# Optimization experiments

Hardware: AMD Instinct MI355X
Metric: run time of the kernel (lower is better)

The kernel has to match this reference:

```python
import jax, jax.numpy as jnp
import numpy as np

EPS = 1e-5

def layer_norm(h, g, b):
    m = h.mean(-1, keepdims=True)
    v = ((h - m) ** 2).mean(-1, keepdims=True)
    return (h - m) * jax.lax.rsqrt(v + EPS) * g + b

def setup_inputs() -> dict:
    key = jax.random.key(0)
    ks = jax.random.split(key, 16)
    B, D, C, H, EH, L = 64, 20000, 16, 64, 128, 32
    s = lambda k, fan_in, shape: jax.random.normal(k, shape, jnp.float32) / np.sqrt(fan_in)
    return {
        "x": jax.random.normal(ks[0], (B, D), jnp.float32),
        "mask": jax.random.randint(ks[1], (B, D), 0, 2, jnp.int32),
        "feature_embedding": jax.random.normal(ks[2], (D, C), jnp.float32),
        # h_layer: Linear(1+C -> H), LN, ReLU, Linear(H -> C), LN, ReLU
        "W1": s(ks[3], 1 + C, (1 + C, H)), "b1": jnp.zeros((H,), jnp.float32),
        "g1": jnp.ones((H,), jnp.float32), "be1": jnp.zeros((H,), jnp.float32),
        "W2": s(ks[4], H, (H, C)), "b2": jnp.zeros((C,), jnp.float32),
        "g2": jnp.ones((C,), jnp.float32), "be2": jnp.zeros((C,), jnp.float32),
        # encoder_mlp (FCLayers, 2 layers, LayerNorm + ReLU each): C -> EH -> 2L
        "We1": s(ks[5], C, (C, EH)), "bb1": jnp.zeros((EH,), jnp.float32),
        "gg1": jnp.ones((EH,), jnp.float32), "bbe1": jnp.zeros((EH,), jnp.float32),
        "We2": s(ks[6], EH, (EH, 2 * L)), "bb2": jnp.zeros((2 * L,), jnp.float32),
        "gg2": jnp.ones((2 * L,), jnp.float32), "bbe2": jnp.zeros((2 * L,), jnp.float32),
    }

def reference(x, mask, feature_embedding, W1, b1, g1, be1, W2, b2, g2, be2,
              We1, bb1, gg1, bbe1, We2, bb2, gg2, bbe2):
    B, D = x.shape
    C = feature_embedding.shape[1]
    # per-feature point-net: h_layer runs row-wise, so we compute it densely
    # for all (b, d) and zero out unobserved entries before pooling —
    # identical math to the per-sample masked gather in the original.
    h_in = jnp.concatenate(
        [x[..., None], jnp.broadcast_to(feature_embedding, (B, D, C))], axis=-1
    )  # [B, D, 1+C]
    h = jax.nn.relu(layer_norm(h_in @ W1 + b1, g1, be1))   # [B, D, H]
    h = jax.nn.relu(layer_norm(h @ W2 + b2, g2, be2))      # [B, D, C]
    m = mask.astype(h.dtype)
    summed = jnp.einsum('bdc,bd->bc', h, m)                # masked sum pool
    num_obs = jnp.maximum(m.sum(axis=1, keepdims=True), 1.0)
    c = summed / num_obs                                   # pool_mode='mean'
    # encoder_mlp
    e = jax.nn.relu(layer_norm(c @ We1 + bb1, gg1, bbe1))
    e = jax.nn.relu(layer_norm(e @ We2 + bb2, gg2, bbe2))  # [B, 2*latent]
    mu, logvar = jnp.split(e, 2, axis=-1)
    return mu, logvar
```

## Files before the change

kernel.cpp:

```cpp
#include <hip/hip_runtime.h>
#include <hip/hip_bf16.h>

#define EPSF 1e-5f

namespace {
constexpr int B = 64, D = 20000, C = 16, H = 64, EH = 128, L = 32;
constexpr int DPAD = ((D + 63) / 64) * 64;
constexpr int NB = 1280;
constexpr int SSTRIDE = NB * 4;
constexpr int FB = 14;
constexpr int MAXU = B * (DPAD / 64);
}

typedef __attribute__((ext_vector_type(8))) short bf16x8;
typedef __attribute__((ext_vector_type(4))) float f32x4;
typedef __attribute__((ext_vector_type(2))) float f32x2;
typedef __attribute__((ext_vector_type(4))) unsigned int u32x4;

static __device__ __forceinline__ unsigned short f2bf(float f) {
    __hip_bfloat16 h = __float2bfloat16(f);
    return __builtin_bit_cast(unsigned short, h);
}
static __device__ __forceinline__ unsigned int packbf(float lo, float hi) {
    return ((unsigned int)f2bf(hi) << 16) | (unsigned int)f2bf(lo);
}
static __device__ __forceinline__ unsigned int cvtpk(float lo, float hi) {
    __hip_bfloat162 h2 = __float22bfloat162_rn(make_float2(lo, hi));
    return ((unsigned int)__builtin_bit_cast(unsigned short, h2.y) << 16)
         | (unsigned int)__builtin_bit_cast(unsigned short, h2.x);
}
static __device__ __forceinline__ f32x2 pk_fma(f32x2 a, f32x2 b, f32x2 c) {
    return __builtin_elementwise_fma(a, b, c);
}
static __device__ __forceinline__ f32x2 pk_add(f32x2 a, f32x2 b) { return a + b; }
static __device__ __forceinline__ f32x2 pk_mul(f32x2 a, f32x2 b) { return a * b; }

__global__ __launch_bounds__(1024) void k_prep(
    const int* __restrict__ mask, const float* __restrict__ x,
    const float* __restrict__ fe,
    const float* __restrict__ W1, const float* __restrict__ b1,
    const float* __restrict__ W2,
    int* __restrict__ cnt,
    unsigned short* __restrict__ cd, unsigned int* __restrict__ hxp,
    unsigned short* __restrict__ febf,
    unsigned short* __restrict__ W1T, unsigned short* __restrict__ W2T)
{
    const int t = threadIdx.x;
    if (blockIdx.x < B) {
        const int b = blockIdx.x;
        const size_t bD = (size_t)b * D;
        const size_t bP = (size_t)b * DPAD;
        constexpr int NIT = (D + 1023) / 1024;
        int   mv[NIT];
        float xv[NIT];
        #pragma unroll
        for (int it = 0; it < NIT; ++it) {
            const int d = it * 1024 + t;
            const bool in = d < D;
            mv[it] = in ? mask[bD + d] : 0;
            xv[it] = in ? x[bD + d] : 0.f;
        }
        int cl = 0;
        #pragma unroll
        for (int it = 0; it < NIT; ++it) cl += (mv[it] != 0) ? 1 : 0;

        const int lane = t & 63, wid = t >> 6;
        int inc = cl;
        #pragma unroll
        for (int off = 1; off < 64; off <<= 1) {
            const int v = __shfl_up(inc, off);
            if (lane >= off) inc += v;
        }
        __shared__ int ls[16];
        if (lane == 63) ls[wid] = inc;
        __syncthreads();
        int wbase = 0, tot = 0;
        #pragma unroll
        for (int k = 0; k < 16; ++k) {
            const int v = ls[k];
            tot += v;
            if (k < wid) wbase += v;
        }
        int pos = wbase + (inc - cl);

        #pragma unroll
        for (int it = 0; it < NIT; ++it) {
            if (mv[it]) {
                cd[bP + pos]  = (unsigned short)(it * 1024 + t);
                hxp[bP + pos] = packbf(xv[it], 1.0f);
                ++pos;
            }
        }
        const int padend = (tot + 63) & ~63;
        for (int i = tot + t; i < padend; i += 1024) {
            cd[bP + i] = 0;
            hxp[bP + i] = 0u;
        }
        if (t == 0) cnt[b] = tot;
    } else if (blockIdx.x == B) {
        for (int e = t; e < H * 32; e += 1024) {
            const int rIdx = e >> 5, kk = e & 31;
            const int m = rIdx >> 4, rho = rIdx & 15;
            const int h = 32 * (m >> 1) + 8 * (rho >> 2) + 4 * (m & 1) + (rho & 3);
            float v = 0.f;
            if (kk < 16)       v = W1[(kk + 1) * H + h];
            else if (kk == 16) v = W1[h];
            else if (kk == 17) v = b1[h];
            W1T[e] = f2bf(v);
        }
    } else if (blockIdx.x == B + 1) {
        for (int e = t; e < C * H; e += 1024) {
            const int c0 = e >> 6, hh = e & 63;
            W2T[e] = f2bf(W2[hh * C + c0]);
        }
    } else {
        const int pb = blockIdx.x - (B + 2);
        for (int u = pb * 1024 + t; u < (D * C) / 8; u += FB * 1024) {
            const float4 f0 = *(const float4*)(fe + (size_t)u * 8);
            const float4 f1 = *(const float4*)(fe + (size_t)u * 8 + 4);
            uint4 pk;
            pk.x = packbf(f0.x, f0.y); pk.y = packbf(f0.z, f0.w);
            pk.z = packbf(f1.x, f1.y); pk.w = packbf(f1.z, f1.w);
            *(uint4*)(febf + (size_t)u * 8) = pk;
        }
    }
}

static __device__ __forceinline__ void unit_it(
    const bf16x8& hbv, int rem, int pq,
    const bf16x8 (&w1f)[4], const bf16x8 (&w2f)[2],
    const f32x2 (&g1p)[4][2], const f32x2 (&be1p)[4][2],
    const f32x2& g2lo, const f32x2& g2hi,
    const f32x2& be2lo, const f32x2& be2hi,
    const f32x2& b2lo, const f32x2& b2hi,
    f32x2& laccLo, f32x2& laccHi)
{
    const f32x4 z = {0.f, 0.f, 0.f, 0.f};
    f32x4 t1a[4];
    #pragma unroll
    for (int m = 0; m < 4; ++m)
        t1a[m] = __builtin_amdgcn_mfma_f32_16x16x32_bf16(w1f[m], hbv, z, 0, 0, 0);

    f32x2 sp = {0.f, 0.f}, qp = {0.f, 0.f};
    f32x2 tl[4], th[4];
    #pragma unroll
    for (int m = 0; m < 4; ++m) {
        tl[m] = __builtin_shufflevector(t1a[m], t1a[m], 0, 1);
        th[m] = __builtin_shufflevector(t1a[m], t1a[m], 2, 3);
        sp = pk_add(sp, pk_add(tl[m], th[m]));
        qp = pk_fma(tl[m], tl[m], pk_fma(th[m], th[m], qp));
    }
    float s  = sp[0] + sp[1];
    float sq = qp[0] + qp[1];
    s  += __shfl_xor(s, 16);  sq += __shfl_xor(sq, 16);
    s  += __shfl_xor(s, 32);  sq += __shfl_xor(sq, 32);
    const float mean1 = s * (1.f / H);
    const float var1  = fmaxf(sq * (1.f / H) - mean1 * mean1, 0.f);
    const float rstd1 = rsqrtf(var1 + EPSF);

    const f32x2 rr2 = {rstd1, rstd1};
    const f32x2 nm2 = {-mean1, -mean1};
    unsigned int pw[8];
    #pragma unroll
    for (int m = 0; m < 4; ++m) {
        const f32x2 sgl = pk_mul(g1p[m][0], rr2);
        const f32x2 sgh = pk_mul(g1p[m][1], rr2);
        const f32x2 obl = pk_fma(sgl, nm2, be1p[m][0]);
        const f32x2 obh = pk_fma(sgh, nm2, be1p[m][1]);
        const f32x2 yl = pk_fma(tl[m], sgl, obl);
        const f32x2 yh = pk_fma(th[m], sgh, obh);
        pw[2 * m]     = cvtpk(fmaxf(yl[0], 0.f), fmaxf(yl[1], 0.f));
        pw[2 * m + 1] = cvtpk(fmaxf(yh[0], 0.f), fmaxf(yh[1], 0.f));
    }
    const u32x4 r0 = {pw[0], pw[1], pw[2], pw[3]};
    const u32x4 r1 = {pw[4], pw[5], pw[6], pw[7]};
    const bf16x8 rb0 = __builtin_bit_cast(bf16x8, r0);
    const bf16x8 rb1 = __builtin_bit_cast(bf16x8, r1);

    f32x4 a2 = __builtin_amdgcn_mfma_f32_16x16x32_bf16(w2f[0], rb0, z, 0, 0, 0);
    a2 = __builtin_amdgcn_mfma_f32_16x16x32_bf16(w2f[1], rb1, a2, 0, 0, 0);

    f32x2 alo = __builtin_shufflevector(a2, a2, 0, 1);
    f32x2 ahi = __builtin_shufflevector(a2, a2, 2, 3);
    alo = pk_add(alo, b2lo);
    ahi = pk_add(ahi, b2hi);
    const f32x2 sp2 = pk_add(alo, ahi);
    const f32x2 zz = {0.f, 0.f};
    const f32x2 qp2 = pk_fma(alo, alo, pk_fma(ahi, ahi, zz));
    float s2 = sp2[0] + sp2[1];
    float q2 = qp2[0] + qp2[1];
    s2 += __shfl_xor(s2, 16);  q2 += __shfl_xor(q2, 16);
    s2 += __shfl_xor(s2, 32);  q2 += __shfl_xor(q2, 32);
    const float mean2 = s2 * (1.f / C);
    const float var2  = fmaxf(q2 * (1.f / C) - mean2 * mean2, 0.f);
    const float rstd2 = rsqrtf(var2 + EPSF);

    const f32x2 rrb = {rstd2, rstd2};
    const f32x2 nmb = {-mean2, -mean2};
    const f32x2 sg2l = pk_mul(g2lo, rrb);
    const f32x2 sg2h = pk_mul(g2hi, rrb);
    const f32x2 ob2l = pk_fma(sg2l, nmb, be2lo);
    const f32x2 ob2h = pk_fma(sg2h, nmb, be2hi);
    const f32x2 y2l = pk_fma(alo, sg2l, ob2l);
    const f32x2 y2h = pk_fma(ahi, sg2h, ob2h);
    const float vm = (pq < rem) ? 1.f : 0.f;
    const f32x2 vm2 = {vm, vm};
    const f32x2 rl = {fmaxf(y2l[0], 0.f), fmaxf(y2l[1], 0.f)};
    const f32x2 rh = {fmaxf(y2h[0], 0.f), fmaxf(y2h[1], 0.f)};
    laccLo = pk_fma(rl, vm2, laccLo);
    laccHi = pk_fma(rh, vm2, laccHi);
}

__global__ __launch_bounds__(256, 2) void k_rows(
    const int* __restrict__ cnt,
    const unsigned short* __restrict__ cd, const unsigned int* __restrict__ hxp,
    const unsigned short* __restrict__ febf,
    const unsigned short* __restrict__ W1T, const unsigned short* __restrict__ W2T,
    const float* __restrict__ g1, const float* __restrict__ be1,
    const float* __restrict__ g2, const float* __restrict__ be2,
    const float* __restrict__ b2,
    float* __restrict__ part)
{
    const int tid = threadIdx.x;
    const int w = tid >> 6, lane = tid & 63;
    const int g = lane >> 4, q = lane & 15;

    const int cv  = cnt[lane];
    const int nuv = (cv + 63) >> 6;
    int Pi = nuv;
    #pragma unroll
    for (int off = 1; off < 64; off <<= 1) {
        const int pv = __shfl_up(Pi, off);
        if (lane >= off) Pi += pv;
    }
    const int T = __shfl(Pi, 63);

    const int uA = blockIdx.x * 4 + w;
    if (uA >= T) return;
    const bool hasB = (uA + SSTRIDE) < T;
    const int uB = hasB ? uA + SSTRIDE : uA;

    bf16x8 w1f[4];
    #pragma unroll
    for (int m = 0; m < 4; ++m)
        w1f[m] = *(const bf16x8*)(W1T + (16 * m + q) * 32 + 8 * g);
    bf16x8 w2f[2];
    #pragma unroll
    for (int ks = 0; ks < 2; ++ks)
        w2f[ks] = *(const bf16x8*)(W2T + q * 64 + 32 * ks + 8 * g);

    f32x2 g1p[4][2], be1p[4][2];
    #pragma unroll
    for (int m = 0; m < 4; ++m) {
        const int h0 = 32 * (m >> 1) + 8 * g + 4 * (m & 1);
        g1p[m][0]  = *(const f32x2*)(g1  + h0);
        g1p[m][1]  = *(const f32x2*)(g1  + h0 + 2);
        be1p[m][0] = *(const f32x2*)(be1 + h0);
        be1p[m][1] = *(const f32x2*)(be1 + h0 + 2);
    }
    const f32x2 g2lo  = *(const f32x2*)(g2  + 4 * g);
    const f32x2 g2hi  = *(const f32x2*)(g2  + 4 * g + 2);
    const f32x2 be2lo = *(const f32x2*)(be2 + 4 * g);
    const f32x2 be2hi = *(const f32x2*)(be2 + 4 * g + 2);
    const f32x2 b2lo  = *(const f32x2*)(b2  + 4 * g);
    const f32x2 b2hi  = *(const f32x2*)(b2  + 4 * g + 2);

    size_t rowbA, rowbB;
    int remA, remB;
    {
        const unsigned long long blA = __ballot(Pi <= uA);
        const int bA   = __popcll(blA);
        const int PbA  = __shfl(Pi, bA);
        const int nubA = __shfl(nuv, bA);
        const int nA   = __shfl(cv, bA);
        const int baseA = (uA - (PbA - nubA)) * 64;
        rowbA = (size_t)bA * DPAD + baseA;
        remA  = nA - baseA;
        const unsigned long long blB = __ballot(Pi <= uB);
        const int bB   = __popcll(blB);
        const int PbB  = __shfl(Pi, bB);
        const int nubB = __shfl(nuv, bB);
        const int nB   = __shfl(cv, bB);
        const int baseB = (uB - (PbB - nubB)) * 64;
        rowbB = (size_t)bB * DPAD + baseB;
        remB  = nB - baseB;
    }

    const int dvA = (int)cd[rowbA + lane];
    const int dvB = (int)cd[rowbB + lane];

    bf16x8 hbA[4], hbB[4];
    #pragma unroll
    for (int it = 0; it < 4; ++it) {
        const int p = (it << 4) + q;
        {
            const int dd = __shfl(dvA, p);
            bf16x8 hv = {0, 0, 0, 0, 0, 0, 0, 0};
            if (g < 2) {
                hv = *(const bf16x8*)(febf + (size_t)dd * 16 + 8 * g);
            } else if (g == 2) {
                const unsigned int xv = hxp[rowbA + p];
                const u32x4 tmp = {xv, 0u, 0u, 0u};
                hv = __builtin_bit_cast(bf16x8, tmp);
            }
            hbA[it] = hv;
        }
        {
            const int dd = __shfl(dvB, p);
            bf16x8 hv = {0, 0, 0, 0, 0, 0, 0, 0};
            if (g < 2) {
                hv = *(const bf16x8*)(febf + (size_t)dd * 16 + 8 * g);
            } else if (g == 2) {
                const unsigned int xv = hxp[rowbB + p];
                const u32x4 tmp = {xv, 0u, 0u, 0u};
                hv = __builtin_bit_cast(bf16x8, tmp);
            }
            hbB[it] = hv;
        }
    }

    f32x2 laLoA = {0.f, 0.f}, laHiA = {0.f, 0.f};
    f32x2 laLoB = {0.f, 0.f}, laHiB = {0.f, 0.f};
    #pragma unroll
    for (int it = 0; it < 4; ++it) {
        const int pq = (it << 4) + q;
        unit_it(hbA[it], remA, pq, w1f, w2f, g1p, be1p,
                g2lo, g2hi, be2lo, be2hi, b2lo, b2hi, laLoA, laHiA);
        unit_it(hbB[it], remB, pq, w1f, w2f, g1p, be1p,
                g2lo, g2hi, be2lo, be2hi, b2lo, b2hi, laLoB, laHiB);
    }

    float a0 = laLoA[0], a1 = laLoA[1], a2 = laHiA[0], a3 = laHiA[1];
    float b0 = laLoB[0], b1 = laLoB[1], b2v_ = laHiB[0], b3 = laHiB[1];
    #pragma unroll
    for (int off = 1; off < 16; off <<= 1) {
        a0 += __shfl_xor(a0, off);  a1 += __shfl_xor(a1, off);
        a2 += __shfl_xor(a2, off);  a3 += __shfl_xor(a3, off);
        b0 += __shfl_xor(b0, off);  b1 += __shfl_xor(b1, off);
        b2v_ += __shfl_xor(b2v_, off);  b3 += __shfl_xor(b3, off);
    }
    if (q == 0) {
        *(float4*)(part + (size_t)uA * C + 4 * g) = make_float4(a0, a1, a2, a3);
        if (hasB)
            *(float4*)(part + (size_t)uB * C + 4 * g) = make_float4(b0, b1, b2v_, b3);
    }
}

__global__ __launch_bounds__(EH) void k_enc(
    const float* __restrict__ part, const int* __restrict__ cnt,
    const float* __restrict__ We1, const float* __restrict__ bb1,
    const float* __restrict__ gg1, const float* __restrict__ bbe1,
    const float* __restrict__ We2, const float* __restrict__ bb2,
    const float* __restrict__ gg2, const float* __restrict__ bbe2,
    float* __restrict__ out)
{
    const int b = blockIdx.x;
    const int t = threadIdx.x;
    __shared__ int sP[64];
    __shared__ float red[8][16];
    __shared__ float cc[C];
    __shared__ float stats[2];
    __shared__ float buf[EH];
    __shared__ float buf2[2 * L];

    if (t < 64) {
        int p = (cnt[t] + 63) >> 6;
        #pragma unroll
        for (int off = 1; off < 64; off <<= 1) {
            const int pv = __shfl_up(p, off);
            if (t >= off) p += pv;
        }
        sP[t] = p;
    }
    __syncthreads();
    const int n = cnt[b];
    const int row0 = (b == 0) ? 0 : sP[b - 1];
    const int rows = sP[b] - row0;

    {
        const int c = t & 15, s = t >> 4;
        float ps = 0.f;
        for (int r = s; r < rows; r += 8)
            ps += part[(size_t)(row0 + r) * C + c];
        red[s][c] = ps;
    }
    __syncthreads();
    if (t < C) {
        float v = 0.f;
        #pragma unroll
        for (int s = 0; s < 8; ++s) v += red[s][t];
        cc[t] = v;
    }
    __syncthreads();
    const float inv = 1.f / fmaxf((float)n, 1.f);

    float v1 = bb1[t];
    #pragma unroll
    for (int c = 0; c < C; ++c)
        v1 = fmaf(cc[c] * inv, We1[c * EH + t], v1);
    buf[t] = v1;
    __syncthreads();
    if (t == 0) {
        float s = 0.f, ss = 0.f;
        for (int j2 = 0; j2 < EH; ++j2) { s += buf[j2]; ss = fmaf(buf[j2], buf[j2], ss); }
        float mn = s * (1.f / EH);
        float vr = fmaxf(ss * (1.f / EH) - mn * mn, 0.f);
        stats[0] = mn; stats[1] = rsqrtf(vr + EPSF);
    }
    __syncthreads();
    float e1 = fmaxf(fmaf((v1 - stats[0]) * stats[1], gg1[t], bbe1[t]), 0.f);
    __syncthreads();
    buf[t] = e1;
    __syncthreads();

    float v2 = 0.f;
    if (t < 2 * L) {
        v2 = bb2[t];
        #pragma unroll
        for (int h = 0; h < EH; ++h)
            v2 = fmaf(buf[h], We2[h * (2 * L) + t], v2);
        buf2[t] = v2;
    }
    __syncthreads();
    if (t == 0) {
        float s = 0.f, ss = 0.f;
        for (int j2 = 0; j2 < 2 * L; ++j2) { s += buf2[j2]; ss = fmaf(buf2[j2], buf2[j2], ss); }
        float mn = s * (1.f / (2 * L));
        float vr = fmaxf(ss * (1.f / (2 * L)) - mn * mn, 0.f);
        stats[0] = mn; stats[1] = rsqrtf(vr + EPSF);
    }
    __syncthreads();
    if (t < 2 * L) {
        float e2 = fmaxf(fmaf((v2 - stats[0]) * stats[1], gg2[t], bbe2[t]), 0.f);
        if (t < L) out[(size_t)b * L + t]                       = e2;
        else       out[(size_t)B * L + (size_t)b * L + (t - L)] = e2;
    }
}

extern "C" void kernel_launch(void* const* d_in, const int* in_sizes, int n_in,
                              void* d_out, int out_size, void* d_ws, size_t ws_size,
                              hipStream_t stream) {
    const float* x    = (const float*)d_in[0];
    const int*   mask = (const int*)d_in[1];
    const float* fe   = (const float*)d_in[2];
    const float* W1   = (const float*)d_in[3];
    const float* b1   = (const float*)d_in[4];
    const float* g1   = (const float*)d_in[5];
    const float* be1  = (const float*)d_in[6];
    const float* W2   = (const float*)d_in[7];
    const float* b2   = (const float*)d_in[8];
    const float* g2   = (const float*)d_in[9];
    const float* be2  = (const float*)d_in[10];
    const float* We1  = (const float*)d_in[11];
    const float* bb1  = (const float*)d_in[12];
    const float* gg1  = (const float*)d_in[13];
    const float* bbe1 = (const float*)d_in[14];
    const float* We2  = (const float*)d_in[15];
    const float* bb2  = (const float*)d_in[16];
    const float* gg2  = (const float*)d_in[17];
    const float* bbe2 = (const float*)d_in[18];
    float* out = (float*)d_out;

    char* wp = (char*)d_ws;
    float* part     = (float*)wp;               wp += (size_t)MAXU * C * 4;
    int*   cnt      = (int*)wp;                 wp += (size_t)B * 4;
    unsigned short* W1T = (unsigned short*)wp;  wp += (size_t)H * 32 * 2;
    unsigned short* W2T = (unsigned short*)wp;  wp += (size_t)C * H * 2;
    unsigned short* febf = (unsigned short*)wp; wp += (size_t)D * C * 2;
    unsigned int*   hxp = (unsigned int*)wp;    wp += (size_t)B * DPAD * 4;
    unsigned short* cd  = (unsigned short*)wp;

    hipLaunchKernelGGL(k_prep, dim3(B + 2 + FB), dim3(1024), 0, stream,
                       mask, x, fe, W1, b1, W2, cnt, cd, hxp, febf, W1T, W2T);
    hipLaunchKernelGGL(k_rows, dim3(NB), dim3(256), 0, stream,
                       cnt, cd, hxp, febf, W1T, W2T, g1, be1, g2, be2, b2, part);
    hipLaunchKernelGGL(k_enc, dim3(B), dim3(EH), 0, stream,
                       part, cnt, We1, bb1, gg1, bbe1, We2, bb2, gg2, bbe2, out);
}
```

Measured before the change: 47.67 us.

## Fuse prep, row, and encoder kernels into one persistent kernel with grid barriers

Merges the three kernel launches into a single persistent kernel of 512 blocks separated by two atomic-counter grid barriers, removing launch gaps between stages. The compaction stage now runs with 256-thread blocks using a ballot-based iterative scan instead of 1024-thread blocks. The row stage loops over units grid-stride instead of one-shot. It adds a memset launch, spin-wait overhead, and relies on all 512 blocks being co-resident (launch bounds allow 2 per CU). The per-batch compaction is now serialized over 79 iterations per block, which could lengthen the first stage.

```diff
diff --git a/kernel.cpp b/kernel.cpp
--- a/kernel.cpp
+++ b/kernel.cpp
@@ -6,9 +6,8 @@
 namespace {
 constexpr int B = 64, D = 20000, C = 16, H = 64, EH = 128, L = 32;
 constexpr int DPAD = ((D + 63) / 64) * 64;
-constexpr int NB = 1280;
-constexpr int SSTRIDE = NB * 4;
-constexpr int FB = 14;
+constexpr int NBF = 512;
+constexpr int WSTRIDE = NBF * 4;
 constexpr int MAXU = B * (DPAD / 64);
 }
 
@@ -35,95 +34,19 @@
 static __device__ __forceinline__ f32x2 pk_add(f32x2 a, f32x2 b) { return a + b; }
 static __device__ __forceinline__ f32x2 pk_mul(f32x2 a, f32x2 b) { return a * b; }
 
-__global__ __launch_bounds__(1024) void k_prep(
-    const int* __restrict__ mask, const float* __restrict__ x,
-    const float* __restrict__ fe,
-    const float* __restrict__ W1, const float* __restrict__ b1,
-    const float* __restrict__ W2,
-    int* __restrict__ cnt,
-    unsigned short* __restrict__ cd, unsigned int* __restrict__ hxp,
-    unsigned short* __restrict__ febf,
-    unsigned short* __restrict__ W1T, unsigned short* __restrict__ W2T)
-{
-    const int t = threadIdx.x;
-    if (blockIdx.x < B) {
-        const int b = blockIdx.x;
-        const size_t bD = (size_t)b * D;
-        const size_t bP = (size_t)b * DPAD;
-        constexpr int NIT = (D + 1023) / 1024;
-        int   mv[NIT];
-        float xv[NIT];
-        #pragma unroll
-        for (int it = 0; it < NIT; ++it) {
-            const int d = it * 1024 + t;
-            const bool in = d < D;
-            mv[it] = in ? mask[bD + d] : 0;
-            xv[it] = in ? x[bD + d] : 0.f;
-        }
-        int cl = 0;
-        #pragma unroll
-        for (int it = 0; it < NIT; ++it) cl += (mv[it] != 0) ? 1 : 0;
-
-        const int lane = t & 63, wid = t >> 6;
-        int inc = cl;
-        #pragma unroll
-        for (int off = 1; off < 64; off <<= 1) {
-            const int v = __shfl_up(inc, off);
-            if (lane >= off) inc += v;
-        }
-        __shared__ int ls[16];
-        if (lane == 63) ls[wid] = inc;
-        __syncthreads();
-        int wbase = 0, tot = 0;
-        #pragma unroll
-        for (int k = 0; k < 16; ++k) {
-            const int v = ls[k];
-            tot += v;
-            if (k < wid) wbase += v;
-        }
-        int pos = wbase + (inc - cl);
-
-        #pragma unroll
-        for (int it = 0; it < NIT; ++it) {
-            if (mv[it]) {
-                cd[bP + pos]  = (unsigned short)(it * 1024 + t);
-                hxp[bP + pos] = packbf(xv[it], 1.0f);
-                ++pos;
-            }
-        }
-        const int padend = (tot + 63) & ~63;
-        for (int i = tot + t; i < padend; i += 1024) {
-            cd[bP + i] = 0;
-            hxp[bP + i] = 0u;
-        }
-        if (t == 0) cnt[b] = tot;
-    } else if (blockIdx.x == B) {
-        for (int e = t; e < H * 32; e += 1024) {
-            const int rIdx = e >> 5, kk = e & 31;
-            const int m = rIdx >> 4, rho = rIdx & 15;
-            const int h = 32 * (m >> 1) + 8 * (rho >> 2) + 4 * (m & 1) + (rho & 3);
-            float v = 0.f;
-            if (kk < 16)       v = W1[(kk + 1) * H + h];
-            else if (kk == 16) v = W1[h];
-            else if (kk == 17) v = b1[h];
-            W1T[e] = f2bf(v);
-        }
-    } else if (blockIdx.x == B + 1) {
-        for (int e = t; e < C * H; e += 1024) {
-            const int c0 = e >> 6, hh = e & 63;
-            W2T[e] = f2bf(W2[hh * C + c0]);
-        }
-    } else {
-        const int pb = blockIdx.x - (B + 2);
-        for (int u = pb * 1024 + t; u < (D * C) / 8; u += FB * 1024) {
-            const float4 f0 = *(const float4*)(fe + (size_t)u * 8);
-            const float4 f1 = *(const float4*)(fe + (size_t)u * 8 + 4);
-            uint4 pk;
-            pk.x = packbf(f0.x, f0.y); pk.y = packbf(f0.z, f0.w);
-            pk.z = packbf(f1.x, f1.y); pk.w = packbf(f1.z, f1.w);
-            *(uint4*)(febf + (size_t)u * 8) = pk;
-        }
-    }
+static __device__ __forceinline__ void grid_barrier(int* bar, int target) {
+    __syncthreads();
+    if (threadIdx.x == 0) {
+        __threadfence();
+        atomicAdd(bar, 1);
+        int spins = 0;
+        while (atomicAdd(bar, 0) < target) {
+            __builtin_amdgcn_s_sleep(8);
+            if (++spins > (1 << 24)) break;
+        }
+        __threadfence();
+    }
+    __syncthreads();
 }
 
 static __device__ __forceinline__ void unit_it(
@@ -211,229 +134,311 @@
     laccHi = pk_fma(rh, vm2, laccHi);
 }
 
-__global__ __launch_bounds__(256, 2) void k_rows(
-    const int* __restrict__ cnt,
-    const unsigned short* __restrict__ cd, const unsigned int* __restrict__ hxp,
-    const unsigned short* __restrict__ febf,
-    const unsigned short* __restrict__ W1T, const unsigned short* __restrict__ W2T,
+__global__ __launch_bounds__(256, 2) void k_fused(
+    const int* __restrict__ mask, const float* __restrict__ x,
+    const float* __restrict__ fe,
+    const float* __restrict__ W1, const float* __restrict__ b1,
     const float* __restrict__ g1, const float* __restrict__ be1,
+    const float* __restrict__ W2, const float* __restrict__ b2,
     const float* __restrict__ g2, const float* __restrict__ be2,
-    const float* __restrict__ b2,
-    float* __restrict__ part)
-{
-    const int tid = threadIdx.x;
-    const int w = tid >> 6, lane = tid & 63;
-    const int g = lane >> 4, q = lane & 15;
-
-    const int cv  = cnt[lane];
-    const int nuv = (cv + 63) >> 6;
-    int Pi = nuv;
-    #pragma unroll
-    for (int off = 1; off < 64; off <<= 1) {
-        const int pv = __shfl_up(Pi, off);
-        if (lane >= off) Pi += pv;
-    }
-    const int T = __shfl(Pi, 63);
-
-    const int uA = blockIdx.x * 4 + w;
-    if (uA >= T) return;
-    const bool hasB = (uA + SSTRIDE) < T;
-    const int uB = hasB ? uA + SSTRIDE : uA;
-
-    bf16x8 w1f[4];
-    #pragma unroll
-    for (int m = 0; m < 4; ++m)
-        w1f[m] = *(const bf16x8*)(W1T + (16 * m + q) * 32 + 8 * g);
-    bf16x8 w2f[2];
-    #pragma unroll
-    for (int ks = 0; ks < 2; ++ks)
-        w2f[ks] = *(const bf16x8*)(W2T + q * 64 + 32 * ks + 8 * g);
-
-    f32x2 g1p[4][2], be1p[4][2];
-    #pragma unroll
-    for (int m = 0; m < 4; ++m) {
-        const int h0 = 32 * (m >> 1) + 8 * g + 4 * (m & 1);
-        g1p[m][0]  = *(const f32x2*)(g1  + h0);
-        g1p[m][1]  = *(const f32x2*)(g1  + h0 + 2);
-        be1p[m][0] = *(const f32x2*)(be1 + h0);
-        be1p[m][1] = *(const f32x2*)(be1 + h0 + 2);
-    }
-    const f32x2 g2lo  = *(const f32x2*)(g2  + 4 * g);
-    const f32x2 g2hi  = *(const f32x2*)(g2  + 4 * g + 2);
-    const f32x2 be2lo = *(const f32x2*)(be2 + 4 * g);
-    const f32x2 be2hi = *(const f32x2*)(be2 + 4 * g + 2);
-    const f32x2 b2lo  = *(const f32x2*)(b2  + 4 * g);
-    const f32x2 b2hi  = *(const f32x2*)(b2  + 4 * g + 2);
-
-    size_t rowbA, rowbB;
-    int remA, remB;
-    {
-        const unsigned long long blA = __ballot(Pi <= uA);
-        const int bA   = __popcll(blA);
-        const int PbA  = __shfl(Pi, bA);
-        const int nubA = __shfl(nuv, bA);
-        const int nA   = __shfl(cv, bA);
-        const int baseA = (uA - (PbA - nubA)) * 64;
-        rowbA = (size_t)bA * DPAD + baseA;
-        remA  = nA - baseA;
-        const unsigned long long blB = __ballot(Pi <= uB);
-        const int bB   = __popcll(blB);
-        const int PbB  = __shfl(Pi, bB);
-        const int nubB = __shfl(nuv, bB);
-        const int nB   = __shfl(cv, bB);
-        const int baseB = (uB - (PbB - nubB)) * 64;
-        rowbB = (size_t)bB * DPAD + baseB;
-        remB  = nB - baseB;
-    }
-
-    const int dvA = (int)cd[rowbA + lane];
-    const int dvB = (int)cd[rowbB + lane];
-
-    bf16x8 hbA[4], hbB[4];
-    #pragma unroll
-    for (int it = 0; it < 4; ++it) {
-        const int p = (it << 4) + q;
-        {
-            const int dd = __shfl(dvA, p);
-            bf16x8 hv = {0, 0, 0, 0, 0, 0, 0, 0};
-            if (g < 2) {
-                hv = *(const bf16x8*)(febf + (size_t)dd * 16 + 8 * g);
-            } else if (g == 2) {
-                const unsigned int xv = hxp[rowbA + p];
-                const u32x4 tmp = {xv, 0u, 0u, 0u};
-                hv = __builtin_bit_cast(bf16x8, tmp);
-            }
-            hbA[it] = hv;
-        }
-        {
-            const int dd = __shfl(dvB, p);
-            bf16x8 hv = {0, 0, 0, 0, 0, 0, 0, 0};
-            if (g < 2) {
-                hv = *(const bf16x8*)(febf + (size_t)dd * 16 + 8 * g);
-            } else if (g == 2) {
-                const unsigned int xv = hxp[rowbB + p];
-                const u32x4 tmp = {xv, 0u, 0u, 0u};
-                hv = __builtin_bit_cast(bf16x8, tmp);
-            }
-            hbB[it] = hv;
-        }
-    }
-
-    f32x2 laLoA = {0.f, 0.f}, laHiA = {0.f, 0.f};
-    f32x2 laLoB = {0.f, 0.f}, laHiB = {0.f, 0.f};
-    #pragma unroll
-    for (int it = 0; it < 4; ++it) {
-        const int pq = (it << 4) + q;
-        unit_it(hbA[it], remA, pq, w1f, w2f, g1p, be1p,
-                g2lo, g2hi, be2lo, be2hi, b2lo, b2hi, laLoA, laHiA);
-        unit_it(hbB[it], remB, pq, w1f, w2f, g1p, be1p,
-                g2lo, g2hi, be2lo, be2hi, b2lo, b2hi, laLoB, laHiB);
-    }
-
-    float a0 = laLoA[0], a1 = laLoA[1], a2 = laHiA[0], a3 = laHiA[1];
-    float b0 = laLoB[0], b1 = laLoB[1], b2v_ = laHiB[0], b3 = laHiB[1];
-    #pragma unroll
-    for (int off = 1; off < 16; off <<= 1) {
-        a0 += __shfl_xor(a0, off);  a1 += __shfl_xor(a1, off);
-        a2 += __shfl_xor(a2, off);  a3 += __shfl_xor(a3, off);
-        b0 += __shfl_xor(b0, off);  b1 += __shfl_xor(b1, off);
-        b2v_ += __shfl_xor(b2v_, off);  b3 += __shfl_xor(b3, off);
-    }
-    if (q == 0) {
-        *(float4*)(part + (size_t)uA * C + 4 * g) = make_float4(a0, a1, a2, a3);
-        if (hasB)
-            *(float4*)(part + (size_t)uB * C + 4 * g) = make_float4(b0, b1, b2v_, b3);
-    }
-}
-
-__global__ __launch_bounds__(EH) void k_enc(
-    const float* __restrict__ part, const int* __restrict__ cnt,
     const float* __restrict__ We1, const float* __restrict__ bb1,
     const float* __restrict__ gg1, const float* __restrict__ bbe1,
     const float* __restrict__ We2, const float* __restrict__ bb2,
     const float* __restrict__ gg2, const float* __restrict__ bbe2,
+    int* __restrict__ cnt, unsigned short* __restrict__ cd,
+    unsigned int* __restrict__ hxp, unsigned short* __restrict__ febf,
+    unsigned short* __restrict__ W1T, unsigned short* __restrict__ W2T,
+    float* __restrict__ part, int* __restrict__ bar,
     float* __restrict__ out)
 {
-    const int b = blockIdx.x;
+    const int bid = blockIdx.x;
     const int t = threadIdx.x;
-    __shared__ int sP[64];
-    __shared__ float red[8][16];
-    __shared__ float cc[C];
-    __shared__ float stats[2];
-    __shared__ float buf[EH];
-    __shared__ float buf2[2 * L];
-
-    if (t < 64) {
-        int p = (cnt[t] + 63) >> 6;
+    const int lane = t & 63, w = t >> 6;
+
+    __shared__ int wc[4];
+
+    if (bid < B) {
+        const int b = bid;
+        const size_t bD = (size_t)b * D;
+        const size_t bP = (size_t)b * DPAD;
+        constexpr int NITC = (D + 255) / 256;
+        int base = 0;
+        int   mv = (t < D) ? mask[bD + t] : 0;
+        float xv = (t < D) ? x[bD + t] : 0.f;
+        for (int it = 0; it < NITC; ++it) {
+            int mv_n = 0; float xv_n = 0.f;
+            const int dn = (it + 1) * 256 + t;
+            if (it + 1 < NITC && dn < D) { mv_n = mask[bD + dn]; xv_n = x[bD + dn]; }
+            const unsigned long long bal = __ballot(mv != 0);
+            if (lane == 0) wc[w] = __popcll(bal);
+            __syncthreads();
+            int woff = 0, tot = 0;
+            #pragma unroll
+            for (int k = 0; k < 4; ++k) {
+                const int c0 = wc[k];
+                tot += c0;
+                if (k < w) woff += c0;
+            }
+            if (mv) {
+                const int pre = __popcll(bal & ((1ull << lane) - 1ull));
+                const int pos = base + woff + pre;
+                cd[bP + pos]  = (unsigned short)(it * 256 + t);
+                hxp[bP + pos] = packbf(xv, 1.0f);
+            }
+            base += tot;
+            __syncthreads();
+            mv = mv_n; xv = xv_n;
+        }
+        const int padend = (base + 63) & ~63;
+        for (int i = base + t; i < padend; i += 256) {
+            cd[bP + i] = 0;
+            hxp[bP + i] = 0u;
+        }
+        if (t == 0) cnt[b] = base;
+    } else if (bid == B) {
+        for (int e = t; e < H * 32; e += 256) {
+            const int rIdx = e >> 5, kk = e & 31;
+            const int m = rIdx >> 4, rho = rIdx & 15;
+            const int h = 32 * (m >> 1) + 8 * (rho >> 2) + 4 * (m & 1) + (rho & 3);
+            float v = 0.f;
+            if (kk < 16)       v = W1[(kk + 1) * H + h];
+            else if (kk == 16) v = W1[h];
+            else if (kk == 17) v = b1[h];
+            W1T[e] = f2bf(v);
+        }
+    } else if (bid == B + 1) {
+        for (int e = t; e < C * H; e += 256) {
+            const int c0 = e >> 6, hh = e & 63;
+            W2T[e] = f2bf(W2[hh * C + c0]);
+        }
+    } else {
+        const int pb = bid - (B + 2);
+        for (int u = pb * 256 + t; u < (D * C) / 8; u += (NBF - B - 2) * 256) {
+            const float4 f0 = *(const float4*)(fe + (size_t)u * 8);
+            const float4 f1 = *(const float4*)(fe + (size_t)u * 8 + 4);
+            uint4 pk;
+            pk.x = packbf(f0.x, f0.y); pk.y = packbf(f0.z, f0.w);
+            pk.z = packbf(f1.x, f1.y); pk.w = packbf(f1.z, f1.w);
+            *(uint4*)(febf + (size_t)u * 8) = pk;
+        }
+    }
+
+    grid_barrier(bar, NBF);
+
+    {
+        const int g = lane >> 4, q = lane & 15;
+
+        const int cv  = cnt[lane];
+        const int nuv = (cv + 63) >> 6;
+        int Pi = nuv;
         #pragma unroll
         for (int off = 1; off < 64; off <<= 1) {
-            const int pv = __shfl_up(p, off);
-            if (t >= off) p += pv;
-        }
-        sP[t] = p;
-    }
-    __syncthreads();
-    const int n = cnt[b];
-    const int row0 = (b == 0) ? 0 : sP[b - 1];
-    const int rows = sP[b] - row0;
-
-    {
-        const int c = t & 15, s = t >> 4;
-        float ps = 0.f;
-        for (int r = s; r < rows; r += 8)
-            ps += part[(size_t)(row0 + r) * C + c];
-        red[s][c] = ps;
-    }
-    __syncthreads();
-    if (t < C) {
-        float v = 0.f;
+            const int pv = __shfl_up(Pi, off);
+            if (lane >= off) Pi += pv;
+        }
+        const int T = __shfl(Pi, 63);
+
+        bf16x8 w1f[4];
         #pragma unroll
-        for (int s = 0; s < 8; ++s) v += red[s][t];
-        cc[t] = v;
-    }
-    __syncthreads();
-    const float inv = 1.f / fmaxf((float)n, 1.f);
-
-    float v1 = bb1[t];
-    #pragma unroll
-    for (int c = 0; c < C; ++c)
-        v1 = fmaf(cc[c] * inv, We1[c * EH + t], v1);
-    buf[t] = v1;
-    __syncthreads();
-    if (t == 0) {
-        float s = 0.f, ss = 0.f;
-        for (int j2 = 0; j2 < EH; ++j2) { s += buf[j2]; ss = fmaf(buf[j2], buf[j2], ss); }
-        float mn = s * (1.f / EH);
-        float vr = fmaxf(ss * (1.f / EH) - mn * mn, 0.f);
-        stats[0] = mn; stats[1] = rsqrtf(vr + EPSF);
-    }
-    __syncthreads();
-    float e1 = fmaxf(fmaf((v1 - stats[0]) * stats[1], gg1[t], bbe1[t]), 0.f);
-    __syncthreads();
-    buf[t] = e1;
-    __syncthreads();
-
-    float v2 = 0.f;
-    if (t < 2 * L) {
-        v2 = bb2[t];
+        for (int m = 0; m < 4; ++m)
+            w1f[m] = *(const bf16x8*)(W1T + (16 * m + q) * 32 + 8 * g);
+        bf16x8 w2f[2];
         #pragma unroll
-        for (int h = 0; h < EH; ++h)
-            v2 = fmaf(buf[h], We2[h * (2 * L) + t], v2);
-        buf2[t] = v2;
-    }
-    __syncthreads();
-    if (t == 0) {
-        float s = 0.f, ss = 0.f;
-        for (int j2 = 0; j2 < 2 * L; ++j2) { s += buf2[j2]; ss = fmaf(buf2[j2], buf2[j2], ss); }
-        float mn = s * (1.f / (2 * L));
-        float vr = fmaxf(ss * (1.f / (2 * L)) - mn * mn, 0.f);
-        stats[0] = mn; stats[1] = rsqrtf(vr + EPSF);
-    }
-    __syncthreads();
-    if (t < 2 * L) {
-        float e2 = fmaxf(fmaf((v2 - stats[0]) * stats[1], gg2[t], bbe2[t]), 0.f);
-        if (t < L) out[(size_t)b * L + t]                       = e2;
-        else       out[(size_t)B * L + (size_t)b * L + (t - L)] = e2;
+        for (int ks = 0; ks < 2; ++ks)
+            w2f[ks] = *(const bf16x8*)(W2T + q * 64 + 32 * ks + 8 * g);
+
+        f32x2 g1p[4][2], be1p[4][2];
+        #pragma unroll
+        for (int m = 0; m < 4; ++m) {
+            const int h0 = 32 * (m >> 1) + 8 * g + 4 * (m & 1);
+            g1p[m][0]  = *(const f32x2*)(g1  + h0);
+            g1p[m][1]  = *(const f32x2*)(g1  + h0 + 2);
+            be1p[m][0] = *(const f32x2*)(be1 + h0);
+            be1p[m][1] = *(const f32x2*)(be1 + h0 + 2);
+        }
+        const f32x2 g2lo  = *(const f32x2*)(g2  + 4 * g);
+        const f32x2 g2hi  = *(const f32x2*)(g2  + 4 * g + 2);
+        const f32x2 be2lo = *(const f32x2*)(be2 + 4 * g);
+        const f32x2 be2hi = *(const f32x2*)(be2 + 4 * g + 2);
+        const f32x2 b2lo  = *(const f32x2*)(b2  + 4 * g);
+        const f32x2 b2hi  = *(const f32x2*)(b2  + 4 * g + 2);
+
+        const int gw = bid * 4 + w;
+        for (int u0 = gw; u0 < T; u0 += 2 * WSTRIDE) {
+            const int uA = u0;
+            const bool hasB_ = (u0 + WSTRIDE) < T;
+            const int uB = hasB_ ? u0 + WSTRIDE : uA;
+
+            size_t rowbA, rowbB;
+            int remA, remB;
+            {
+                const unsigned long long blA = __ballot(Pi <= uA);
+                const int bA   = __popcll(blA);
+                const int PbA  = __shfl(Pi, bA);
+                const int nubA = __shfl(nuv, bA);
+                const int nA   = __shfl(cv, bA);
+                const int baseA = (uA - (PbA - nubA)) * 64;
+                rowbA = (size_t)bA * DPAD + baseA;
+                remA  = nA - baseA;
+                const unsigned long long blB = __ballot(Pi <= uB);
+                const int bB   = __popcll(blB);
+                const int PbB  = __shfl(Pi, bB);
+                const int nubB = __shfl(nuv, bB);
+                const int nB   = __shfl(cv, bB);
+                const int baseB = (uB - (PbB - nubB)) * 64;
+                rowbB = (size_t)bB * DPAD + baseB;
+                remB  = nB - baseB;
+            }
+
+            const int dvA = (int)cd[rowbA + lane];
+            const int dvB = (int)cd[rowbB + lane];
+
+            bf16x8 hbA[4], hbB[4];
+            #pragma unroll
+            for (int it = 0; it < 4; ++it) {
+                const int p = (it << 4) + q;
+                {
+                    const int dd = __shfl(dvA, p);
+                    bf16x8 hv = {0, 0, 0, 0, 0, 0, 0, 0};
+                    if (g < 2) {
+                        hv = *(const bf16x8*)(febf + (size_t)dd * 16 + 8 * g);
+                    } else if (g == 2) {
+                        const unsigned int xv2 = hxp[rowbA + p];
+                        const u32x4 tmp = {xv2, 0u, 0u, 0u};
+                        hv = __builtin_bit_cast(bf16x8, tmp);
+                    }
+                    hbA[it] = hv;
+                }
+                {
+                    const int dd = __shfl(dvB, p);
+                    bf16x8 hv = {0, 0, 0, 0, 0, 0, 0, 0};
+                    if (g < 2) {
+                        hv = *(const bf16x8*)(febf + (size_t)dd * 16 + 8 * g);
+                    } else if (g == 2) {
+                        const unsigned int xv2 = hxp[rowbB + p];
+                        const u32x4 tmp = {xv2, 0u, 0u, 0u};
+                        hv = __builtin_bit_cast(bf16x8, tmp);
+                    }
+                    hbB[it] = hv;
+                }
+            }
+
+            f32x2 laLoA = {0.f, 0.f}, laHiA = {0.f, 0.f};
+            f32x2 laLoB = {0.f, 0.f}, laHiB = {0.f, 0.f};
+            #pragma unroll
+            for (int it = 0; it < 4; ++it) {
+                const int pq = (it << 4) + q;
+                unit_it(hbA[it], remA, pq, w1f, w2f, g1p, be1p,
+                        g2lo, g2hi, be2lo, be2hi, b2lo, b2hi, laLoA, laHiA);
+                unit_it(hbB[it], remB, pq, w1f, w2f, g1p, be1p,
+                        g2lo, g2hi, be2lo, be2hi, b2lo, b2hi, laLoB, laHiB);
+            }
+
+            float a0 = laLoA[0], a1 = laLoA[1], a2 = laHiA[0], a3 = laHiA[1];
+            float b0 = laLoB[0], b1v = laLoB[1], b2v_ = laHiB[0], b3 = laHiB[1];
+            #pragma unroll
+            for (int off = 1; off < 16; off <<= 1) {
+                a0 += __shfl_xor(a0, off);  a1 += __shfl_xor(a1, off);
+                a2 += __shfl_xor(a2, off);  a3 += __shfl_xor(a3, off);
+                b0 += __shfl_xor(b0, off);  b1v += __shfl_xor(b1v, off);
+                b2v_ += __shfl_xor(b2v_, off);  b3 += __shfl_xor(b3, off);
+            }
+            if (q == 0) {
+                *(float4*)(part + (size_t)uA * C + 4 * g) = make_float4(a0, a1, a2, a3);
+                if (hasB_)
+                    *(float4*)(part + (size_t)uB * C + 4 * g) = make_float4(b0, b1v, b2v_, b3);
+            }
+        }
+    }
+
+    grid_barrier(bar, 2 * NBF);
+
+    if (bid < B) {
+        const int b = bid;
+        __shared__ int sP[64];
+        __shared__ float red[8][16];
+        __shared__ float cc[C];
+        __shared__ float stats[2];
+        __shared__ float buf[EH];
+        __shared__ float buf2[2 * L];
+
+        if (t < 64) {
+            int p = (cnt[t] + 63) >> 6;
+            #pragma unroll
+            for (int off = 1; off < 64; off <<= 1) {
+                const int pv = __shfl_up(p, off);
+                if (t >= off) p += pv;
+            }
+            sP[t] = p;
+        }
+        __syncthreads();
+        const int n = cnt[b];
+        const int row0 = (b == 0) ? 0 : sP[b - 1];
+        const int rows = sP[b] - row0;
+
+        if (t < 128) {
+            const int c = t & 15, s = t >> 4;
+            float ps = 0.f;
+            for (int r = s; r < rows; r += 8)
+                ps += part[(size_t)(row0 + r) * C + c];
+            red[s][c] = ps;
+        }
+        __syncthreads();
+        if (t < C) {
+            float v = 0.f;
+            #pragma unroll
+            for (int s = 0; s < 8; ++s) v += red[s][t];
+            cc[t] = v;
+        }
+        __syncthreads();
+        const float inv = 1.f / fmaxf((float)n, 1.f);
+
+        float v1 = 0.f;
+        if (t < EH) {
+            v1 = bb1[t];
+            #pragma unroll
+            for (int c = 0; c < C; ++c)
+                v1 = fmaf(cc[c] * inv, We1[c * EH + t], v1);
+            buf[t] = v1;
+        }
+        __syncthreads();
+        if (t == 0) {
+            float s = 0.f, ss = 0.f;
+            for (int j2 = 0; j2 < EH; ++j2) { s += buf[j2]; ss = fmaf(buf[j2], buf[j2], ss); }
+            float mn = s * (1.f / EH);
+            float vr = fmaxf(ss * (1.f / EH) - mn * mn, 0.f);
+            stats[0] = mn; stats[1] = rsqrtf(vr + EPSF);
+        }
+        __syncthreads();
+        float e1 = 0.f;
+        if (t < EH)
+            e1 = fmaxf(fmaf((v1 - stats[0]) * stats[1], gg1[t], bbe1[t]), 0.f);
+        __syncthreads();
+        if (t < EH) buf[t] = e1;
+        __syncthreads();
+
+        float v2 = 0.f;
+        if (t < 2 * L) {
+            v2 = bb2[t];
+            #pragma unroll
+            for (int h = 0; h < EH; ++h)
+                v2 = fmaf(buf[h], We2[h * (2 * L) + t], v2);
+            buf2[t] = v2;
+        }
+        __syncthreads();
+        if (t == 0) {
+            float s = 0.f, ss = 0.f;
+            for (int j2 = 0; j2 < 2 * L; ++j2) { s += buf2[j2]; ss = fmaf(buf2[j2], buf2[j2], ss); }
+            float mn = s * (1.f / (2 * L));
+            float vr = fmaxf(ss * (1.f / (2 * L)) - mn * mn, 0.f);
+            stats[0] = mn; stats[1] = rsqrtf(vr + EPSF);
+        }
+        __syncthreads();
+        if (t < 2 * L) {
+            float e2 = fmaxf(fmaf((v2 - stats[0]) * stats[1], gg2[t], bbe2[t]), 0.f);
+            if (t < L) out[(size_t)b * L + t]                       = e2;
+            else       out[(size_t)B * L + (size_t)b * L + (t - L)] = e2;
+        }
     }
 }
 
@@ -464,16 +469,16 @@
     char* wp = (char*)d_ws;
     float* part     = (float*)wp;               wp += (size_t)MAXU * C * 4;
     int*   cnt      = (int*)wp;                 wp += (size_t)B * 4;
+    int*   bar      = (int*)wp;                 wp += 64;
     unsigned short* W1T = (unsigned short*)wp;  wp += (size_t)H * 32 * 2;
     unsigned short* W2T = (unsigned short*)wp;  wp += (size_t)C * H * 2;
     unsigned short* febf = (unsigned short*)wp; wp += (size_t)D * C * 2;
     unsigned int*   hxp = (unsigned int*)wp;    wp += (size_t)B * DPAD * 4;
     unsigned short* cd  = (unsigned short*)wp;
 
-    hipLaunchKernelGGL(k_prep, dim3(B + 2 + FB), dim3(1024), 0, stream,
-                       mask, x, fe, W1, b1, W2, cnt, cd, hxp, febf, W1T, W2T);
-    hipLaunchKernelGGL(k_rows, dim3(NB), dim3(256), 0, stream,
-                       cnt, cd, hxp, febf, W1T, W2T, g1, be1, g2, be2, b2, part);
-    hipLaunchKernelGGL(k_enc, dim3(B), dim3(EH), 0, stream,
-                       part, cnt, We1, bb1, gg1, bbe1, We2, bb2, gg2, bbe2, out);
-}
+    hipMemsetAsync(bar, 0, 64, stream);
+    hipLaunchKernelGGL(k_fused, dim3(NBF), dim3(256), 0, stream,
+                       mask, x, fe, W1, b1, g1, be1, W2, b2, g2, be2,
+                       We1, bb1, gg1, bbe1, We2, bb2, gg2, bbe2,
+                       cnt, cd, hxp, febf, W1T, W2T, part, bar, out);
+}
```

New measurement: 153.7 us. 3.23x slower.
